# Kernel optimization log

Measured on AMD Instinct MI355X. Metric: run time of the kernel, lower is better.

## Reference

```python
import jax, jax.numpy as jnp
import numpy as np

N_NODES = 50000
N_EDGES = 640000
D = 128
L = 3


def setup_inputs() -> dict:
    key = jax.random.key(0)
    k1, k2, k3, k4 = jax.random.split(key, 4)
    x = jax.random.normal(k1, (N_NODES, D), dtype=jnp.float32)
    # Glorot-ish scale so activations stay O(1) across 3 layers
    Ws = jax.random.normal(k2, (L, D, D), dtype=jnp.float32) * (1.0 / np.sqrt(D))
    bs = jnp.zeros((L, D), dtype=jnp.float32)
    edge_src = jax.random.randint(k3, (N_EDGES,), 0, N_NODES, dtype=jnp.int32)
    edge_dst = jax.random.randint(k4, (N_EDGES,), 0, N_NODES, dtype=jnp.int32)
    return {"x": x, "Ws": Ws, "bs": bs, "edge_src": edge_src, "edge_dst": edge_dst}


def reference(x, Ws, bs, edge_src, edge_dst):
    n = x.shape[0]
    ones = jnp.ones(edge_src.shape[0], dtype=x.dtype)
    # degrees, clamped to 1 as in dgl GraphConv(norm='both')
    deg_out = jnp.maximum(jax.ops.segment_sum(ones, edge_src, num_segments=n), 1.0)
    deg_in = jnp.maximum(jax.ops.segment_sum(ones, edge_dst, num_segments=n), 1.0)
    inv_sqrt_out = jax.lax.rsqrt(deg_out)[:, None]  # [N,1]
    inv_sqrt_in = jax.lax.rsqrt(deg_in)[:, None]    # [N,1]
    for l in range(Ws.shape[0]):
        h = x * inv_sqrt_out                         # src normalization
        msg = h[edge_src]                            # [E,D] gather
        agg = jax.ops.segment_sum(msg, edge_dst, num_segments=n)  # [N,D] scatter-add
        h = agg * inv_sqrt_in                        # dst normalization
        x = jax.nn.relu(h @ Ws[l] + bs[l])           # linear + ReLU
    return x
```

## Files before the change

### kernel.cpp

```cpp
#include <hip/hip_runtime.h>
#include <hip/hip_fp16.h>

typedef __attribute__((ext_vector_type(8))) _Float16 half8;
typedef __attribute__((ext_vector_type(4))) float f32x4;
typedef unsigned int u32;
typedef unsigned short u16;
typedef unsigned long long u64;

#define ELL_PAD 64
#define BKT 128
#define BKT_SH 7
#define EPB 2048
#define NAMAX 512


__global__ __launch_bounds__(256) void initpack(int* __restrict__ deg_out,
                                                u32* __restrict__ xz0,
                                                u32* __restrict__ xz1,
                                                const float* __restrict__ Ws,
                                                _Float16* __restrict__ Whi,
                                                _Float16* __restrict__ Wlo,
                                                int N, int padU32, int zb, int packTotal) {
  int b = blockIdx.x;
  if (b < zb) {
    int i = b * 256 + threadIdx.x;
    if (i < N) deg_out[i] = 0;
    if (b == 0) {
      for (int j = threadIdx.x; j < padU32; j += 256) { xz0[j] = 0; xz1[j] = 0; }
    }
    return;
  }
  int i = (b - zb) * 256 + threadIdx.x;
  if (i < packTotal) {
    int lane  = i & 63;
    int kstep = (i >> 6) & 3;
    int ntile = (i >> 8) & 7;
    int layer = i >> 11;
    int nn = ntile * 16 + (lane & 15);
    int k0 = kstep * 32 + (lane >> 4) * 8;
    const float* W = Ws + (size_t)layer * 128 * 128;
    size_t base = (size_t)i * 8;
    for (int j = 0; j < 8; j++) {
      float v = W[(k0 + j) * 128 + nn];
      _Float16 hi = (_Float16)v;
      Whi[base + j] = hi;
      Wlo[base + j] = (_Float16)(v - (float)hi);
    }
  }
}


__global__ __launch_bounds__(256) void parta(const int* __restrict__ esrc,
                                             const int* __restrict__ edst,
                                             int* __restrict__ deg_out,
                                             u32* __restrict__ part,
                                             u32* __restrict__ runTab,
                                             int E, int NB) {
  __shared__ u32 hist[1024];
  __shared__ u32 stage[EPB];
  int a = blockIdx.x;
  int e0 = a * EPB;
  int e1 = min(E, e0 + EPB);
  int len = e1 - e0;
  for (int j = threadIdx.x; j <= NB; j += 256) hist[j] = 0;
  __syncthreads();
  for (int i = e0 + threadIdx.x; i < e1; i += 256) {
    int s = esrc[i];
    int d = edst[i];
    atomicAdd(&deg_out[s], 1);
    atomicAdd(&hist[d >> BKT_SH], 1u);
  }
  __syncthreads();
  if (threadIdx.x == 0) {
    u32 run = 0;
    for (int b = 0; b < NB; b++) { u32 t = hist[b]; hist[b] = run; run += t; }
  }
  __syncthreads();
  u32* rt = runTab + (size_t)a * (NB + 1);
  for (int b = threadIdx.x; b < NB; b += 256) rt[b] = hist[b];
  if (threadIdx.x == 0) rt[NB] = (u32)len;
  __syncthreads();
  for (int i = e0 + threadIdx.x; i < e1; i += 256) {
    int s = esrc[i];
    int d = edst[i];
    u32 p = atomicAdd(&hist[d >> BKT_SH], 1u);
    stage[p] = (u32)s | ((u32)(d & (BKT - 1)) << 16);
  }
  __syncthreads();
  u32* op = part + (size_t)a * EPB;
  for (int j = threadIdx.x; j < len; j += 256) op[j] = stage[j];
}


__global__ __launch_bounds__(256) void partb(const u32* __restrict__ part,
                                             const u32* __restrict__ runTab,
                                             int* __restrict__ deg_in,
                                             u16* __restrict__ ell,
                                             int N, int NA, int NB) {
  __shared__ u16 slice[BKT * ELL_PAD];
  __shared__ u32 cnt[BKT];
  __shared__ u32 roff[NAMAX + 1];
  __shared__ u32 rbase[NAMAX];
  int b = blockIdx.x;
  int base = b * BKT;
  int hi = min(BKT, N - base);
  if (hi <= 0) return;

  u32 nv = ((u32)N << 16) | (u32)N;
  u32* s32 = (u32*)slice;
  for (int j = threadIdx.x; j < BKT * (ELL_PAD / 2); j += 256) s32[j] = nv;
  for (int j = threadIdx.x; j < BKT; j += 256) cnt[j] = 0;
  for (int a = threadIdx.x; a < NA; a += 256) {
    u32 s = runTab[(size_t)a * (NB + 1) + b];
    u32 e = runTab[(size_t)a * (NB + 1) + b + 1];
    roff[a]  = e - s;
    rbase[a] = (u32)a * EPB + s;
  }
  __syncthreads();
  if (threadIdx.x == 0) {
    u32 run = 0;
    for (int a = 0; a < NA; a++) { u32 t = roff[a]; roff[a] = run; run += t; }
    roff[NA] = run;
  }
  __syncthreads();
  int T = (int)roff[NA];
  for (int i = threadIdx.x; i < T; i += 256) {
    int lo = 0, hh = NA;
    while (hh - lo > 1) {
      int mid = (lo + hh) >> 1;
      if (roff[mid] <= (u32)i) lo = mid; else hh = mid;
    }
    u32 pair = part[(size_t)rbase[lo] + ((u32)i - roff[lo])];
    u32 dl  = pair >> 16;
    u32 src = pair & 0xFFFFu;
    u32 c = atomicAdd(&cnt[dl], 1u);
    if (c < ELL_PAD) slice[dl * ELL_PAD + c] = (u16)src;
  }
  __syncthreads();
  for (int t = threadIdx.x; t < hi; t += 256) deg_in[base + t] = (int)cnt[t];
  u32* eg = (u32*)(ell + (size_t)base * ELL_PAD);
  for (int j = threadIdx.x; j < hi * (ELL_PAD / 2); j += 256) eg[j] = s32[j];
}


__global__ __launch_bounds__(256) void xscale(const float* __restrict__ x,
                                              const int* __restrict__ deg_out,
                                              __half2* __restrict__ xh, int n64) {
  int gid = blockIdx.x * 256 + threadIdx.x;
  if (gid >= n64) return;
  int row = gid >> 6;
  int d = deg_out[row]; if (d < 1) d = 1;
  float s = rsqrtf((float)d);
  float2 v = ((const float2*)x)[gid];
  xh[gid] = __floats2half2_rn(v.x * s, v.y * s);
}


__global__ __launch_bounds__(512) void layer16(const _Float16* __restrict__ xh,
                                               const int* __restrict__ deg_in,
                                               const u16* __restrict__ ell,
                                               const _Float16* __restrict__ Whi,
                                               const _Float16* __restrict__ Wlo,
                                               const float* __restrict__ bias,
                                               const int* __restrict__ deg_out,
                                               __half* __restrict__ out16,
                                               float* __restrict__ out32, int n) {
  __shared__ _Float16 As[16 * 136];
  const int wave = threadIdx.x >> 6;
  const int lane = threadIdx.x & 63;
  const int sub  = lane & 15;
  const int grp  = lane >> 4;
  const int sh   = grp << 4;
  const u32 sub16 = (u32)sub * 16u;
  const int rowBase = blockIdx.x * 16;
  const char* __restrict__ xb = (const char*)xh;

  {
    int r0 = rowBase + wave * 2, r1 = r0 + 1;
    int d0 = (r0 < n) ? deg_in[r0] : 0;
    int d1 = (r1 < n) ? deg_in[r1] : 0;
    int l0 = d0 > ELL_PAD ? ELL_PAD : d0;
    int l1 = d1 > ELL_PAD ? ELL_PAD : d1;
    int t0 = (l0 + 3) & ~3;
    int t1 = (l1 + 3) & ~3;
    const u16* ep0 = ell + (u32)(r0 < n ? r0 : 0) * ELL_PAD;
    const u16* ep1 = ell + (u32)(r1 < n ? r1 : 0) * ELL_PAD;

    float a0[8] = {0.f, 0.f, 0.f, 0.f, 0.f, 0.f, 0.f, 0.f};
    float a1[8] = {0.f, 0.f, 0.f, 0.f, 0.f, 0.f, 0.f, 0.f};

    int m = t0 < t1 ? t0 : t1;
    int e = 0;
    for (; e + 8 <= m; e += 8) {
      u64 wa0 = *(const u64*)&ep0[e];
      u64 wa1 = *(const u64*)&ep0[e + 4];
      u64 wb0 = *(const u64*)&ep1[e];
      u64 wb1 = *(const u64*)&ep1[e + 4];
      u32 ia0 = ((u32)(wa0 >> sh) & 0xFFFFu) * 256u + sub16;
      u32 ia1 = ((u32)(wa1 >> sh) & 0xFFFFu) * 256u + sub16;
      u32 ib0 = ((u32)(wb0 >> sh) & 0xFFFFu) * 256u + sub16;
      u32 ib1 = ((u32)(wb1 >> sh) & 0xFFFFu) * 256u + sub16;
      half8 va0 = *(const half8*)(xb + ia0);
      half8 va1 = *(const half8*)(xb + ia1);
      half8 vb0 = *(const half8*)(xb + ib0);
      half8 vb1 = *(const half8*)(xb + ib1);
#pragma unroll
      for (int j = 0; j < 8; j++) {
        a0[j] += (float)va0[j] + (float)va1[j];
        a1[j] += (float)vb0[j] + (float)vb1[j];
      }
    }
    for (; e < m; e += 4) {
      u64 wa = *(const u64*)&ep0[e];
      u64 wb = *(const u64*)&ep1[e];
      u32 ia = ((u32)(wa >> sh) & 0xFFFFu) * 256u + sub16;
      u32 ib = ((u32)(wb >> sh) & 0xFFFFu) * 256u + sub16;
      half8 va = *(const half8*)(xb + ia);
      half8 vb = *(const half8*)(xb + ib);
#pragma unroll
      for (int j = 0; j < 8; j++) { a0[j] += (float)va[j]; a1[j] += (float)vb[j]; }
    }
    for (int ea = m; ea < t0; ea += 4) {
      u64 wa = *(const u64*)&ep0[ea];
      u32 ia = ((u32)(wa >> sh) & 0xFFFFu) * 256u + sub16;
      half8 va = *(const half8*)(xb + ia);
#pragma unroll
      for (int j = 0; j < 8; j++) a0[j] += (float)va[j];
    }
    for (int eb = m; eb < t1; eb += 4) {
      u64 wb = *(const u64*)&ep1[eb];
      u32 ib = ((u32)(wb >> sh) & 0xFFFFu) * 256u + sub16;
      half8 vb = *(const half8*)(xb + ib);
#pragma unroll
      for (int j = 0; j < 8; j++) a1[j] += (float)vb[j];
    }

#pragma unroll
    for (int j = 0; j < 8; j++) {
      a0[j] += __shfl_xor(a0[j], 16, 64);
      a0[j] += __shfl_xor(a0[j], 32, 64);
      a1[j] += __shfl_xor(a1[j], 16, 64);
      a1[j] += __shfl_xor(a1[j], 32, 64);
    }

    float si0 = rsqrtf((float)(d0 < 1 ? 1 : d0));
    float si1 = rsqrtf((float)(d1 < 1 ? 1 : d1));
    if (grp == 0) {
      half8 h0, h1;
#pragma unroll
      for (int j = 0; j < 8; j++) {
        h0[j] = (_Float16)(a0[j] * si0);
        h1[j] = (_Float16)(a1[j] * si1);
      }
      *(half8*)&As[(wave * 2 + 0) * 136 + sub * 8] = h0;
      *(half8*)&As[(wave * 2 + 1) * 136 + sub * 8] = h1;
    }
  }
  __syncthreads();

  f32x4 acc = (f32x4){0.f, 0.f, 0.f, 0.f};
#pragma unroll
  for (int ks = 0; ks < 4; ks++) {
    half8 a  = *(const half8*)&As[(size_t)sub * 136 + ks * 32 + grp * 8];
    half8 bh = *(const half8*)&Whi[((wave * 4 + ks) * 64 + lane) * 8];
    half8 bl = *(const half8*)&Wlo[((wave * 4 + ks) * 64 + lane) * 8];
    acc = __builtin_amdgcn_mfma_f32_16x16x32_f16(a, bh, acc, 0, 0, 0);
    acc = __builtin_amdgcn_mfma_f32_16x16x32_f16(a, bl, acc, 0, 0, 0);
  }

  const int r0c = rowBase + grp * 4;
  const int col = wave * 16 + sub;
  const float bv = bias[col];
#pragma unroll
  for (int r = 0; r < 4; r++) {
    int row = r0c + r;
    if (row < n) {
      float v = fmaxf(acc[r] + bv, 0.f);
      if (out16) {
        int d = deg_out[row]; if (d < 1) d = 1;
        out16[(size_t)row * 128 + col] = __float2half(v * rsqrtf((float)d));
      } else {
        out32[(size_t)row * 128 + col] = v;
      }
    }
  }
}


extern "C" void kernel_launch(void* const* d_in, const int* in_sizes, int n_in,
                              void* d_out, int out_size, void* d_ws, size_t ws_size,
                              hipStream_t stream) {
  const float* x   = (const float*)d_in[0];
  const float* Ws  = (const float*)d_in[1];
  const float* bs  = (const float*)d_in[2];
  const int* esrc  = (const int*)d_in[3];
  const int* edst  = (const int*)d_in[4];

  const int D = 128;
  const int N = in_sizes[0] / D;
  const int E = in_sizes[3];
  const int L = in_sizes[1] / (D * D);
  const int Npad = ((N + 15) / 16) * 16;
  const int NA = (E + EPB - 1) / EPB;
  const int NB = (N + BKT - 1) / BKT;

  char* base = (char*)d_ws;
  size_t off = 0;
  auto alloc = [&](size_t bytes) {
    char* p = base + off;
    off = (off + bytes + 255) & ~(size_t)255;
    return p;
  };
  int*      deg_out = (int*)alloc((size_t)N * 4);
  int*      deg_in  = (int*)alloc((size_t)N * 4);
  u16*      ell     = (u16*)alloc((size_t)N * ELL_PAD * 2);
  _Float16* Whi     = (_Float16*)alloc((size_t)L * 16384 * 2);
  _Float16* Wlo     = (_Float16*)alloc((size_t)L * 16384 * 2);
  _Float16* xh0     = (_Float16*)alloc((size_t)(Npad + 16) * 128 * 2);
  _Float16* xh1     = (_Float16*)alloc((size_t)(Npad + 16) * 128 * 2);
  u32*      part    = (u32*)alloc((size_t)NA * EPB * 4);
  u32*      runTab  = (u32*)alloc((size_t)NA * (NB + 1) * 4);

  const int zb = (N + 255) / 256;
  const int packTotal = L * 2048;
  const int packB = (packTotal + 255) / 256;
  const int padU32 = 16 * 64;

  initpack<<<dim3(zb + packB), dim3(256), 0, stream>>>(
      deg_out,
      (u32*)(xh0 + (size_t)N * 128), (u32*)(xh1 + (size_t)N * 128),
      Ws, Whi, Wlo, N, padU32, zb, packTotal);
  parta<<<dim3(NA), dim3(256), 0, stream>>>(
      esrc, edst, deg_out, part, runTab, E, NB);
  partb<<<dim3(NB), dim3(256), 0, stream>>>(
      part, runTab, deg_in, ell, N, NA, NB);
  xscale<<<dim3((N * 64 + 255) / 256), dim3(256), 0, stream>>>(
      x, deg_out, (__half2*)xh0, N * 64);

  float* outf = (float*)d_out;
  _Float16* ping[2] = {xh0, xh1};
  const dim3 lgrid(Npad / 16), lblk(512);

  for (int l = 0; l < L; l++) {
    bool last = (l == L - 1);
    layer16<<<lgrid, lblk, 0, stream>>>(
        (const _Float16*)ping[l & 1], deg_in, ell,
        Whi + (size_t)l * 16384, Wlo + (size_t)l * 16384,
        bs + (size_t)l * D, deg_out,
        last ? nullptr : (__half*)ping[(l + 1) & 1],
        last ? outf : nullptr, N);
  }
}
```

Baseline: 250.8 us.

## Parallelize partition scans and sort ELL neighbors by source bucket

The partition kernels move to 512 threads and replace serial single-thread prefix sums with parallel Hillis-Steele scans. partb drops the per-edge binary search for most edges by using a shared run-id table, and stages the edge pairs in shared memory. It then does a two-pass counting sort that orders each destination's ELL neighbor list by source high bits, likely to improve gather locality in the layer kernels. The cost is extra shared memory, a second pass and more barriers, with a binary-search fallback for buckets beyond the staging capacity.

```diff
diff --git a/kernel.cpp b/kernel.cpp
--- a/kernel.cpp
+++ b/kernel.cpp
@@ -12,6 +12,7 @@
 #define BKT_SH 7
 #define EPB 2048
 #define NAMAX 512
+#define RUNCAP 3072
 
 
 __global__ __launch_bounds__(256) void initpack(int* __restrict__ deg_out,
@@ -50,37 +51,44 @@
 }
 
 
-__global__ __launch_bounds__(256) void parta(const int* __restrict__ esrc,
+__global__ __launch_bounds__(512) void parta(const int* __restrict__ esrc,
                                              const int* __restrict__ edst,
                                              int* __restrict__ deg_out,
                                              u32* __restrict__ part,
                                              u32* __restrict__ runTab,
                                              int E, int NB) {
-  __shared__ u32 hist[1024];
+  __shared__ u32 hist[512];
   __shared__ u32 stage[EPB];
+  __shared__ u32 scanA[512];
   int a = blockIdx.x;
   int e0 = a * EPB;
   int e1 = min(E, e0 + EPB);
   int len = e1 - e0;
-  for (int j = threadIdx.x; j <= NB; j += 256) hist[j] = 0;
-  __syncthreads();
-  for (int i = e0 + threadIdx.x; i < e1; i += 256) {
+  int tid = threadIdx.x;
+  if (tid <= NB) hist[tid] = 0;
+  __syncthreads();
+  for (int i = e0 + tid; i < e1; i += 512) {
     int s = esrc[i];
     int d = edst[i];
     atomicAdd(&deg_out[s], 1);
     atomicAdd(&hist[d >> BKT_SH], 1u);
   }
   __syncthreads();
-  if (threadIdx.x == 0) {
-    u32 run = 0;
-    for (int b = 0; b < NB; b++) { u32 t = hist[b]; hist[b] = run; run += t; }
-  }
-  __syncthreads();
+  u32 myc = (tid < NB) ? hist[tid] : 0;
+  scanA[tid] = myc;
+  __syncthreads();
+  for (int off = 1; off < NB; off <<= 1) {
+    u32 t = scanA[tid] + ((tid >= off) ? scanA[tid - off] : 0);
+    __syncthreads();
+    scanA[tid] = t;
+    __syncthreads();
+  }
+  u32 excl = scanA[tid] - myc;
   u32* rt = runTab + (size_t)a * (NB + 1);
-  for (int b = threadIdx.x; b < NB; b += 256) rt[b] = hist[b];
-  if (threadIdx.x == 0) rt[NB] = (u32)len;
-  __syncthreads();
-  for (int i = e0 + threadIdx.x; i < e1; i += 256) {
+  if (tid < NB) { rt[tid] = excl; hist[tid] = excl; }
+  if (tid == 0) rt[NB] = (u32)len;
+  __syncthreads();
+  for (int i = e0 + tid; i < e1; i += 512) {
     int s = esrc[i];
     int d = edst[i];
     u32 p = atomicAdd(&hist[d >> BKT_SH], 1u);
@@ -88,58 +96,98 @@
   }
   __syncthreads();
   u32* op = part + (size_t)a * EPB;
-  for (int j = threadIdx.x; j < len; j += 256) op[j] = stage[j];
-}
-
-
-__global__ __launch_bounds__(256) void partb(const u32* __restrict__ part,
+  for (int j = tid; j < len; j += 512) op[j] = stage[j];
+}
+
+
+__global__ __launch_bounds__(512) void partb(const u32* __restrict__ part,
                                              const u32* __restrict__ runTab,
                                              int* __restrict__ deg_in,
                                              u16* __restrict__ ell,
                                              int N, int NA, int NB) {
   __shared__ u16 slice[BKT * ELL_PAD];
-  __shared__ u32 cnt[BKT];
+  __shared__ u32 cnt2[BKT * 17];
   __shared__ u32 roff[NAMAX + 1];
   __shared__ u32 rbase[NAMAX];
+  __shared__ u16 runid[RUNCAP];
+  __shared__ u32 pstage[RUNCAP];
+  __shared__ u32 scanA[512];
   int b = blockIdx.x;
   int base = b * BKT;
   int hi = min(BKT, N - base);
   if (hi <= 0) return;
+  int tid = threadIdx.x;
 
   u32 nv = ((u32)N << 16) | (u32)N;
   u32* s32 = (u32*)slice;
-  for (int j = threadIdx.x; j < BKT * (ELL_PAD / 2); j += 256) s32[j] = nv;
-  for (int j = threadIdx.x; j < BKT; j += 256) cnt[j] = 0;
-  for (int a = threadIdx.x; a < NA; a += 256) {
-    u32 s = runTab[(size_t)a * (NB + 1) + b];
-    u32 e = runTab[(size_t)a * (NB + 1) + b + 1];
-    roff[a]  = e - s;
-    rbase[a] = (u32)a * EPB + s;
-  }
-  __syncthreads();
-  if (threadIdx.x == 0) {
-    u32 run = 0;
-    for (int a = 0; a < NA; a++) { u32 t = roff[a]; roff[a] = run; run += t; }
-    roff[NA] = run;
-  }
+  for (int j = tid; j < BKT * (ELL_PAD / 2); j += 512) s32[j] = nv;
+  for (int j = tid; j < BKT * 17; j += 512) cnt2[j] = 0;
+  u32 mylen = 0;
+  if (tid < NA) {
+    u32 s = runTab[(size_t)tid * (NB + 1) + b];
+    u32 e = runTab[(size_t)tid * (NB + 1) + b + 1];
+    mylen = e - s;
+    rbase[tid] = (u32)tid * EPB + s;
+  }
+  scanA[tid] = mylen;
+  __syncthreads();
+  for (int off = 1; off < NA + 1; off <<= 1) {
+    u32 t = scanA[tid] + ((tid >= off) ? scanA[tid - off] : 0);
+    __syncthreads();
+    scanA[tid] = t;
+    __syncthreads();
+  }
+  if (tid <= NA) roff[tid] = scanA[tid] - mylen;
   __syncthreads();
   int T = (int)roff[NA];
-  for (int i = threadIdx.x; i < T; i += 256) {
-    int lo = 0, hh = NA;
-    while (hh - lo > 1) {
-      int mid = (lo + hh) >> 1;
-      if (roff[mid] <= (u32)i) lo = mid; else hh = mid;
-    }
-    u32 pair = part[(size_t)rbase[lo] + ((u32)i - roff[lo])];
+  for (int a = tid; a < NA; a += 512) {
+    u32 s0 = roff[a];
+    u32 l  = roff[a + 1] - s0;
+    for (u32 k = 0; k < l; k++)
+      if (s0 + k < RUNCAP) runid[s0 + k] = (u16)a;
+  }
+  __syncthreads();
+  for (int i = tid; i < T; i += 512) {
+    int a;
+    if (i < RUNCAP) a = runid[i];
+    else {
+      int lo = 0, hh = NA;
+      while (hh - lo > 1) { int mid = (lo + hh) >> 1; if (roff[mid] <= (u32)i) lo = mid; else hh = mid; }
+      a = lo;
+    }
+    u32 pair = part[(size_t)rbase[a] + ((u32)i - roff[a])];
+    if (i < RUNCAP) pstage[i] = pair;
     u32 dl  = pair >> 16;
     u32 src = pair & 0xFFFFu;
-    u32 c = atomicAdd(&cnt[dl], 1u);
-    if (c < ELL_PAD) slice[dl * ELL_PAD + c] = (u16)src;
-  }
-  __syncthreads();
-  for (int t = threadIdx.x; t < hi; t += 256) deg_in[base + t] = (int)cnt[t];
+    atomicAdd(&cnt2[dl * 17 + (src >> 12)], 1u);
+  }
+  __syncthreads();
+  if (tid < BKT) {
+    u32 run = 0;
+    for (int bk = 0; bk < 16; bk++) {
+      u32 t = cnt2[tid * 17 + bk];
+      cnt2[tid * 17 + bk] = run;
+      run += t;
+    }
+    if (tid < hi) deg_in[base + tid] = (int)run;
+  }
+  __syncthreads();
+  for (int i = tid; i < T; i += 512) {
+    u32 pair;
+    if (i < RUNCAP) pair = pstage[i];
+    else {
+      int lo = 0, hh = NA;
+      while (hh - lo > 1) { int mid = (lo + hh) >> 1; if (roff[mid] <= (u32)i) lo = mid; else hh = mid; }
+      pair = part[(size_t)rbase[lo] + ((u32)i - roff[lo])];
+    }
+    u32 dl  = pair >> 16;
+    u32 src = pair & 0xFFFFu;
+    u32 p = atomicAdd(&cnt2[dl * 17 + (src >> 12)], 1u);
+    if (p < ELL_PAD) slice[dl * ELL_PAD + p] = (u16)src;
+  }
+  __syncthreads();
   u32* eg = (u32*)(ell + (size_t)base * ELL_PAD);
-  for (int j = threadIdx.x; j < hi * (ELL_PAD / 2); j += 256) eg[j] = s32[j];
+  for (int j = tid; j < hi * (ELL_PAD / 2); j += 512) eg[j] = s32[j];
 }
 
 
@@ -330,9 +378,9 @@
       deg_out,
       (u32*)(xh0 + (size_t)N * 128), (u32*)(xh1 + (size_t)N * 128),
       Ws, Whi, Wlo, N, padU32, zb, packTotal);
-  parta<<<dim3(NA), dim3(256), 0, stream>>>(
+  parta<<<dim3(NA), dim3(512), 0, stream>>>(
       esrc, edst, deg_out, part, runTab, E, NB);
-  partb<<<dim3(NB), dim3(256), 0, stream>>>(
+  partb<<<dim3(NB), dim3(512), 0, stream>>>(
       part, runTab, deg_in, ell, N, NA, NB);
   xscale<<<dim3((N * 64 + 255) / 256), dim3(256), 0, stream>>>(
       x, deg_out, (__half2*)xh0, N * 64);
```

After: 241.6 us. -3.6%, faster.
